# Optimization experiments

Hardware: AMD Instinct MI355X
Metric: run time of the kernel (lower is better)

Reference implementation:

```python
import jax, jax.numpy as jnp
import numpy as np

IMG_H, IMG_W = 512, 512
FEAT_HW = [64, 32, 16, 8, 4]
STRIDES = [8, 16, 32, 64, 128]
IN_CH = 256
NUM_ANCHORS = 9
NUM_CLASSES = 91
SCORE_THRESH = 0.05
NMS_THRESH = 0.5
TOPK = 1000            # batch_size_per_image
DETS = 300             # detections_per_image
BBOX_CLIP = float(np.log(1000.0 / 16.0))
PRIOR_P = 0.01


def _make_anchors():
    # torchvision-style grid anchors, 3 scales x 3 aspect ratios per location
    all_a = []
    for lvl, (hw, stride) in enumerate(zip(FEAT_HW, STRIDES)):
        base = 32.0 * (2.0 ** lvl)
        scales = np.array([1.0, 2.0 ** (1.0 / 3.0), 2.0 ** (2.0 / 3.0)])
        ratios = np.array([0.5, 1.0, 2.0])
        ws = (base * scales[None, :] / np.sqrt(ratios)[:, None]).reshape(-1)  # [9]
        hs = (base * scales[None, :] * np.sqrt(ratios)[:, None]).reshape(-1)
        shifts = (np.arange(hw) + 0.5) * stride
        cy, cx = np.meshgrid(shifts, shifts, indexing='ij')
        cx = cx.reshape(-1, 1)
        cy = cy.reshape(-1, 1)
        a = np.stack([cx - ws / 2, cy - hs / 2, cx + ws / 2, cy + hs / 2], axis=-1)  # [HW, 9, 4]
        all_a.append(a.reshape(-1, 4))
    return np.concatenate(all_a, axis=0).astype(np.float32)


def setup_inputs() -> dict:
    key = jax.random.key(0)
    ks = jax.random.split(key, 10)
    inp = {}
    for i, hw in enumerate(FEAT_HW):
        inp[f'feat{i}'] = jax.random.normal(ks[i], (1, IN_CH, hw, hw), jnp.float32)
    inp['anchors'] = jnp.asarray(_make_anchors())
    tower_std, out_std = 0.03, 0.01
    inp['cls_tower_w'] = jax.random.normal(ks[5], (4, IN_CH, IN_CH, 3, 3), jnp.float32) * tower_std
    inp['cls_tower_b'] = jnp.zeros((4, IN_CH), jnp.float32)
    inp['cls_logits_w'] = jax.random.normal(ks[6], (NUM_ANCHORS * NUM_CLASSES, IN_CH, 3, 3), jnp.float32) * out_std
    inp['cls_logits_b'] = jnp.full((NUM_ANCHORS * NUM_CLASSES,), -np.log((1.0 - PRIOR_P) / PRIOR_P), jnp.float32)
    inp['reg_tower_w'] = jax.random.normal(ks[7], (4, IN_CH, IN_CH, 3, 3), jnp.float32) * tower_std
    inp['reg_tower_b'] = jnp.zeros((4, IN_CH), jnp.float32)
    inp['reg_bbox_w'] = jax.random.normal(ks[8], (NUM_ANCHORS * 4, IN_CH, 3, 3), jnp.float32) * out_std
    inp['reg_bbox_b'] = jnp.zeros((NUM_ANCHORS * 4,), jnp.float32)
    return inp


def _conv3x3(x, w, b):
    y = jax.lax.conv_general_dilated(x, w, (1, 1), 'SAME', dimension_numbers=('NCHW', 'OIHW', 'NCHW'))
    return y + b[None, :, None, None]


def _head(x, tw, tb, ow, ob, out_ch):
    # 4-layer conv tower with ReLU, then output conv; reshape to [B, H*W*A, out_ch]
    for i in range(4):
        x = jax.nn.relu(_conv3x3(x, tw[i], tb[i]))
    y = _conv3x3(x, ow, ob)  # [B, A*out_ch, H, W]
    B, _, H, W = y.shape
    return y.reshape(B, NUM_ANCHORS, out_ch, H, W).transpose(0, 3, 4, 1, 2).reshape(B, H * W * NUM_ANCHORS, out_ch)


def _decode(rel, anc):
    # BoxCoder.decode_single with weights (1,1,1,1)
    w = anc[:, 2] - anc[:, 0]
    h = anc[:, 3] - anc[:, 1]
    cx = anc[:, 0] + 0.5 * w
    cy = anc[:, 1] + 0.5 * h
    dx, dy = rel[:, 0], rel[:, 1]
    dw = jnp.minimum(rel[:, 2], BBOX_CLIP)
    dh = jnp.minimum(rel[:, 3], BBOX_CLIP)
    pcx = dx * w + cx
    pcy = dy * h + cy
    pw = jnp.exp(dw) * w
    ph = jnp.exp(dh) * h
    return jnp.stack([pcx - 0.5 * pw, pcy - 0.5 * ph, pcx + 0.5 * pw, pcy + 0.5 * ph], axis=1)


def _level_candidates(logits, reg, anc):
    # logits [A_l, K], reg [A_l, 4], anc [A_l, 4]
    scores = jax.nn.sigmoid(logits).reshape(-1)          # [A_l*K]
    masked = jnp.where(scores > SCORE_THRESH, scores, -1.0)
    top_s, top_i = jax.lax.top_k(masked, TOPK)           # fixed-size topk; invalid -> -1
    labels = top_i % NUM_CLASSES
    a_idx = top_i // NUM_CLASSES
    boxes = _decode(reg[a_idx], anc[a_idx])
    boxes = jnp.stack([
        jnp.clip(boxes[:, 0], 0.0, float(IMG_W)), jnp.clip(boxes[:, 1], 0.0, float(IMG_H)),
        jnp.clip(boxes[:, 2], 0.0, float(IMG_W)), jnp.clip(boxes[:, 3], 0.0, float(IMG_H))], axis=1)
    return top_s, boxes, labels


def _nms_image(boxes, scores, labels):
    # batched_nms: offset boxes by label so different classes never overlap,
    # then greedy NMS with fixed DETS iterations (padded with invalid slots).
    NEG = jnp.float32(-1e9)
    off = labels.astype(boxes.dtype) * (jnp.max(boxes) + 1.0)
    b = boxes + off[:, None]
    area = (b[:, 2] - b[:, 0]) * (b[:, 3] - b[:, 1])
    alive0 = jnp.where(scores > SCORE_THRESH, scores, NEG)

    def step(alive, _):
        j = jnp.argmax(alive)
        valid = alive[j] > SCORE_THRESH
        bj = b[j]
        lt = jnp.maximum(bj[:2], b[:, :2])
        rb = jnp.minimum(bj[2:], b[:, 2:])
        wh = jnp.maximum(rb - lt, 0.0)
        inter = wh[:, 0] * wh[:, 1]
        iou = inter / (area[j] + area - inter + 1e-12)
        alive = jnp.where(iou > NMS_THRESH, NEG, alive).at[j].set(NEG)
        return alive, (j, valid)

    _, (sel, valid) = jax.lax.scan(step, alive0, None, length=DETS)
    out_s = jnp.where(valid, scores[sel], 0.0)
    out_b = jnp.where(valid[:, None], boxes[sel], 0.0)
    out_l = jnp.where(valid, labels[sel], -1)
    return out_s, out_b, out_l


def _forward(feats, anchors, ctw, ctb, cow, cob, rtw, rtb, row, rob):
    cand = []
    a_off = 0
    for f in feats:
        B, _, H, W = f.shape
        logits = _head(f, ctw, ctb, cow, cob, NUM_CLASSES)   # [B, HWA, K]
        reg = _head(f, rtw, rtb, row, rob, 4)                # [B, HWA, 4]
        a_l = H * W * NUM_ANCHORS
        anc = anchors[a_off:a_off + a_l]
        a_off += a_l
        cand.append(jax.vmap(_level_candidates, in_axes=(0, 0, None))(logits, reg, anc))
    scores = jnp.concatenate([c[0] for c in cand], axis=1)   # [B, 5*TOPK]
    boxes = jnp.concatenate([c[1] for c in cand], axis=1)    # [B, 5*TOPK, 4]
    labels = jnp.concatenate([c[2] for c in cand], axis=1)
    out_s, out_b, out_l = jax.vmap(_nms_image)(boxes, scores, labels)
    out = jnp.concatenate([out_s[..., None], out_b], axis=-1)  # [B, DETS, 5] = (score, x1, y1, x2, y2)
    return out, out_l


def reference(feat0, feat1, feat2, feat3, feat4, anchors, cls_tower_w, cls_tower_b,
              cls_logits_w, cls_logits_b, reg_tower_w, reg_tower_b, reg_bbox_w, reg_bbox_b):
    out, labels = _forward([feat0, feat1, feat2, feat3, feat4], anchors,
                           cls_tower_w, cls_tower_b, cls_logits_w, cls_logits_b,
                           reg_tower_w, reg_tower_b, reg_bbox_w, reg_bbox_b)
    return out, labels
```

## Files before the change

kernel.cpp:

```cpp
#include <hip/hip_runtime.h>
#include <hip/hip_bf16.h>
#include <math.h>

#define CIN 256
#define NUM_CLASSES 91
#define NUM_ANCH 9
#define KEY_CAP 65536
#define NCAND 5000
#define BBOX_CLIP_F 4.135166556742356f
#define CLS_THRESH 0.05f
#define PITCH 5456
#define PP_TOT 5972
#define PLANE_E 1528832
#define PLANE_B 3057664
#define ABUF_B  6115328
#define SLB     147456
#define LO_OFF  13312
#define PHASE   26624

typedef __attribute__((ext_vector_type(4))) float f4;
typedef _Float16 h8 __attribute__((ext_vector_type(8)));

#define MFMA(a,b,c) __builtin_amdgcn_mfma_f32_16x16x32_f16(a,b,c,0,0,0)

__constant__ int c_wsh[5]  = {6,5,4,3,2};
__constant__ int c_hw[5]   = {4096,1024,256,64,16};
__constant__ int c_wp[5]   = {66,34,18,10,6};
__constant__ int c_poff[5] = {0,4356,5512,5836,5936};
__constant__ int c_slen[5] = {198,136,108,100,36};
__constant__ int c_loff[5] = {0,4096,5120,5376,5440};
__constant__ int c_aoff[5] = {0,36864,46080,48384,48960};
__constant__ int s_cum[11] = {0,16,32,48,64,80,96,112,164,168,184};

__device__ __forceinline__ unsigned short f16r(float f) {
    _Float16 h = (_Float16)f;
    return __builtin_bit_cast(unsigned short, h);
}
__device__ __forceinline__ float f16tof(unsigned short u) {
    return (float)__builtin_bit_cast(_Float16, u);
}
__device__ __forceinline__ void split16(float v, unsigned short& h, unsigned short& l) {
    unsigned short hh = (fabsf(v) < 6.103515625e-05f) ? (unsigned short)0 : f16r(v);
    h = hh;
    l = f16r((v - f16tof(hh)) * 4096.0f);
}
__device__ __forceinline__ void gl_lds(const void* g, void* l) {
    __builtin_amdgcn_global_load_lds((const __attribute__((address_space(1))) void*)g,
                                     (__attribute__((address_space(3))) void*)l, 16, 0, 0);
}
__device__ __forceinline__ void tile_geom(int tile, int& lvl, int& px0, int& y0) {
    if (tile < 64)      { lvl = 0; px0 = tile << 6; y0 = tile; }
    else if (tile < 80) { lvl = 1; int j = tile - 64; px0 = j << 6; y0 = j << 1; }
    else if (tile < 84) { lvl = 2; int j = tile - 80; px0 = j << 6; y0 = j << 2; }
    else if (tile == 84){ lvl = 3; px0 = 0; y0 = 0; }
    else                { lvl = 4; px0 = 0; y0 = 0; }
}

__global__ void pad_k(const float* __restrict__ f0, const float* __restrict__ f1,
                      const float* __restrict__ f2, const float* __restrict__ f3,
                      const float* __restrict__ f4, unsigned short* __restrict__ IN) {
    int gid = blockIdx.x * 256 + threadIdx.x;
    if (gid >= 256 * PITCH) return;
    int cin = gid / PITCH, g = gid - cin * PITCH;
    int lvl = (g < 4096) ? 0 : (g < 5120) ? 1 : (g < 5376) ? 2 : (g < 5440) ? 3 : 4;
    const float* f = (lvl == 0) ? f0 : (lvl == 1) ? f1 : (lvl == 2) ? f2 : (lvl == 3) ? f3 : f4;
    int pix = g - c_loff[lvl];
    int wsh = c_wsh[lvl];
    int y = pix >> wsh, x = pix & ((1 << wsh) - 1);
    float v = f[(size_t)cin * c_hw[lvl] + pix];
    unsigned short h, l;
    split16(v, h, l);
    size_t idx = ((size_t)(cin >> 5) * PP_TOT + c_poff[lvl] + (size_t)(y + 1) * c_wp[lvl] + x + 1) * 32 + (cin & 31);
    IN[idx] = h;
    IN[PLANE_E + idx] = l;
}

__global__ void wprep_k(const float* __restrict__ ctw, const float* __restrict__ rtw,
                        const float* __restrict__ cow, const float* __restrict__ row_,
                        unsigned short* __restrict__ wf) {
    int gid = blockIdx.x * 256 + threadIdx.x;
    if (gid >= 184 * 72 * 64) return;
    int lane = gid & 63;
    int t = gid >> 6;
    int tap = t % 9;
    int t2 = t / 9;
    int chunk = t2 & 7;
    int cbg = t2 >> 3;
    int r = 0;
#pragma unroll
    for (int i = 1; i <= 10; ++i) if (cbg >= s_cum[i]) r = i;
    int cbl = cbg - s_cum[r];
    const float* src;
    int coutCnt;
    if (r < 3)       { src = ctw + (size_t)(r + 1) * 589824; coutCnt = 256; }
    else if (r < 7)  { src = rtw + (size_t)(r - 3) * 589824; coutCnt = 256; }
    else if (r == 7) { src = cow; coutCnt = 819; }
    else if (r == 8) { src = row_; coutCnt = 36; }
    else             { src = ctw; coutCnt = 256; }
    int cout = cbl * 16 + (lane & 15);
    int q = lane >> 4;
    unsigned short H[8], L[8];
#pragma unroll
    for (int j = 0; j < 8; ++j) {
        int cin = chunk * 32 + q * 8 + j;
        float v = (cout < coutCnt) ? src[((size_t)cout * 256 + cin) * 9 + tap] : 0.0f;
        split16(v, H[j], L[j]);
    }
    size_t off = (size_t)cbg * 73728 + (size_t)(chunk * 9 + tap) * 1024 + (size_t)lane * 8;
#pragma unroll
    for (int j = 0; j < 8; ++j) { wf[off + j] = H[j]; wf[off + 512 + j] = L[j]; }
}

__device__ __forceinline__ void kloop(const unsigned short* __restrict__ src,
        const char* __restrict__ wf0, char* sm, int wid, int lane,
        int s_base, int s_len, int Wp, const int sloc[2], f4 acc1[2][2], f4 acc2[2][2]) {
    const char* wp = wf0 + lane * 16;
    int nc = (s_len * 64 + 1023) >> 10;
    const char* gbase = (const char*)src;
    {
        const char* g = gbase + (size_t)s_base * 64;
        for (int c = wid; c < nc; c += 4) {
            gl_lds(g + (size_t)c * 1024 + (size_t)lane * 16, sm + c * 1024);
            gl_lds(g + PLANE_B + (size_t)c * 1024 + (size_t)lane * 16, sm + LO_OFF + c * 1024);
        }
    }
    h8 bh0 = *(const h8*)(wp);
    h8 bl0 = *(const h8*)(wp + 1024);
    h8 bh1 = *(const h8*)(wp + SLB);
    h8 bl1 = *(const h8*)(wp + SLB + 1024);
    __syncthreads();
    for (int chunk = 0; chunk < 8; ++chunk) {
        char* smc = sm + (chunk & 1) * PHASE;
        if (chunk < 7) {
            char* smn = sm + ((chunk & 1) ^ 1) * PHASE;
            const char* g = gbase + ((size_t)(chunk + 1) * PP_TOT + s_base) * 64;
            for (int c = wid; c < nc; c += 4) {
                gl_lds(g + (size_t)c * 1024 + (size_t)lane * 16, smn + c * 1024);
                gl_lds(g + PLANE_B + (size_t)c * 1024 + (size_t)lane * 16, smn + LO_OFF + c * 1024);
            }
        }
#pragma unroll
        for (int tap = 0; tap < 9; ++tap) {
            int kt = chunk * 9 + tap;
            int wo2 = ((kt < 71) ? kt + 1 : kt) * 2048;
            h8 nh0 = *(const h8*)(wp + wo2);
            h8 nl0 = *(const h8*)(wp + wo2 + 1024);
            h8 nh1 = *(const h8*)(wp + SLB + wo2);
            h8 nl1 = *(const h8*)(wp + SLB + wo2 + 1024);
            int toff = ((tap / 3) - 1) * Wp + (tap % 3) - 1;
            int so = toff * 64;
            h8 ah0 = *(const h8*)(smc + sloc[0] + so);
            h8 al0 = *(const h8*)(smc + LO_OFF + sloc[0] + so);
            h8 ah1 = *(const h8*)(smc + sloc[1] + so);
            h8 al1 = *(const h8*)(smc + LO_OFF + sloc[1] + so);
            acc1[0][0] = MFMA(ah0, bh0, acc1[0][0]);
            acc2[0][0] = MFMA(al0, bh0, acc2[0][0]);
            acc2[0][0] = MFMA(ah0, bl0, acc2[0][0]);
            acc1[1][0] = MFMA(ah1, bh0, acc1[1][0]);
            acc2[1][0] = MFMA(al1, bh0, acc2[1][0]);
            acc2[1][0] = MFMA(ah1, bl0, acc2[1][0]);
            acc1[0][1] = MFMA(ah0, bh1, acc1[0][1]);
            acc2[0][1] = MFMA(al0, bh1, acc2[0][1]);
            acc2[0][1] = MFMA(ah0, bl1, acc2[0][1]);
            acc1[1][1] = MFMA(ah1, bh1, acc1[1][1]);
            acc2[1][1] = MFMA(al1, bh1, acc2[1][1]);
            acc2[1][1] = MFMA(ah1, bl1, acc2[1][1]);
            bh0 = nh0; bl0 = nl0; bh1 = nh1; bl1 = nl1;
        }
        __syncthreads();
    }
}

__global__ __launch_bounds__(256, 3) void conv_t(
        const unsigned short* __restrict__ srcC, const unsigned short* __restrict__ srcR,
        unsigned short* __restrict__ dstC, unsigned short* __restrict__ dstR,
        const unsigned short* __restrict__ wfC, const unsigned short* __restrict__ wfR,
        const float* __restrict__ bC, const float* __restrict__ bR) {
    __shared__ __align__(16) char sm[2 * PHASE];
    int tid = threadIdx.x, lane = tid & 63, wid = tid >> 6;
    int quad = lane >> 4, l16 = lane & 15;
    int bx = blockIdx.x;
    int cb = bx & 3, tower = (bx >> 2) & 1, tile = bx >> 3;
    const unsigned short* src = tower ? srcR : srcC;
    unsigned short* dst = tower ? dstR : dstC;
    const unsigned short* wfx = tower ? wfR : wfC;
    const float* bias = tower ? bR : bC;

    int lvl, px0, y0;
    tile_geom(tile, lvl, px0, y0);
    int wsh = c_wsh[lvl], HW = c_hw[lvl], Wp = c_wp[lvl];
    int poff = c_poff[lvl];
    int s_base = poff + y0 * Wp, s_len = c_slen[lvl];
    int Mh = (wid & 1) * 32, Nh32 = wid >> 1;

    int sloc[2];
#pragma unroll
    for (int mb = 0; mb < 2; ++mb) {
        int p = px0 + Mh + mb * 16 + l16;
        if (p >= HW) p = HW - 1;
        int y = p >> wsh, x = p & ((1 << wsh) - 1);
        sloc[mb] = ((y - y0 + 1) * Wp + x + 1) * 64 + quad * 16;
    }
    f4 acc1[2][2], acc2[2][2];
#pragma unroll
    for (int mb = 0; mb < 2; ++mb)
#pragma unroll
        for (int sl = 0; sl < 2; ++sl) { acc1[mb][sl] = (f4)0.0f; acc2[mb][sl] = (f4)0.0f; }

    const char* wf0 = (const char*)wfx + (size_t)(cb * 4 + Nh32 * 2) * SLB;
    kloop(src, wf0, sm, wid, lane, s_base, s_len, Wp, sloc, acc1, acc2);

    int cbase = cb * 64 + Nh32 * 32;
    float bv[2];
    bv[0] = bias[cbase + l16];
    bv[1] = bias[cbase + 16 + l16];
#pragma unroll
    for (int mb = 0; mb < 2; ++mb) {
        int pb = px0 + Mh + mb * 16 + quad * 4;
#pragma unroll
        for (int r = 0; r < 4; ++r) {
            int p = pb + r;
            bool valid = p < HW;
            int pc = valid ? p : 0;
            int y = pc >> wsh, x = pc & ((1 << wsh) - 1);
            size_t ppix = poff + (size_t)(y + 1) * Wp + x + 1;
#pragma unroll
            for (int sl = 0; sl < 2; ++sl) {
                int coutg = cbase + sl * 16 + l16;
                float v = fmaf(acc2[mb][sl][r], 0.000244140625f, acc1[mb][sl][r]) + bv[sl];
                v = fmaxf(v, 0.0f);
                unsigned short h, l;
                split16(v, h, l);
                size_t idx = ((size_t)(coutg >> 5) * PP_TOT + ppix) * 32 + (coutg & 31);
                if (valid) { dst[idx] = h; dst[PLANE_E + idx] = l; }
            }
        }
    }
}

__global__ __launch_bounds__(256, 3) void mhead_t(
        const unsigned short* __restrict__ srcC, const unsigned short* __restrict__ srcR,
        const unsigned short* __restrict__ wfCls, const unsigned short* __restrict__ wfReg,
        const float* __restrict__ cob, const float* __restrict__ rob,
        unsigned long long* __restrict__ keys, int* __restrict__ cnt,
        float* __restrict__ regout) {
    __shared__ __align__(16) char sm[2 * PHASE];
    int tid = threadIdx.x, lane = tid & 63, wid = tid >> 6;
    int quad = lane >> 4, l16 = lane & 15;
    int bx = blockIdx.x, tile = bx / 14, sub = bx - tile * 14;
    bool isCls = sub < 13;

    int lvl, px0, y0;
    tile_geom(tile, lvl, px0, y0);
    int wsh = c_wsh[lvl], HW = c_hw[lvl], Wp = c_wp[lvl];
    int poff = c_poff[lvl];
    int s_base = poff + y0 * Wp, s_len = c_slen[lvl];
    int Mh = (wid & 1) * 32, Nh32 = wid >> 1;

    int sloc[2];
#pragma unroll
    for (int mb = 0; mb < 2; ++mb) {
        int p = px0 + Mh + mb * 16 + l16;
        if (p >= HW) p = HW - 1;
        int y = p >> wsh, x = p & ((1 << wsh) - 1);
        sloc[mb] = ((y - y0 + 1) * Wp + x + 1) * 64 + quad * 16;
    }
    f4 acc1[2][2], acc2[2][2];
#pragma unroll
    for (int mb = 0; mb < 2; ++mb)
#pragma unroll
        for (int sl = 0; sl < 2; ++sl) { acc1[mb][sl] = (f4)0.0f; acc2[mb][sl] = (f4)0.0f; }

    const unsigned short* src = isCls ? srcC : srcR;
    const char* wf0 = isCls ? (const char*)wfCls + (size_t)(sub * 4 + Nh32 * 2) * SLB
                            : (const char*)wfReg + (size_t)(Nh32 * 2) * SLB;
    kloop(src, wf0, sm, wid, lane, s_base, s_len, Wp, sloc, acc1, acc2);

    if (isCls) {
        int chb = sub * 64 + Nh32 * 32;
        float cbv[2];
#pragma unroll
        for (int sl = 0; sl < 2; ++sl) {
            int ch = chb + sl * 16 + l16;
            cbv[sl] = (ch < 819) ? cob[ch] : 0.0f;
        }
#pragma unroll
        for (int mb = 0; mb < 2; ++mb) {
            int pb = px0 + Mh + mb * 16 + quad * 4;
#pragma unroll
            for (int r = 0; r < 4; ++r) {
                int p = pb + r;
                bool valid = p < HW;
#pragma unroll
                for (int sl = 0; sl < 2; ++sl) {
                    int ch = chb + sl * 16 + l16;
                    if (valid && ch < 819) {
                        float lg = fmaf(acc2[mb][sl][r], 0.000244140625f, acc1[mb][sl][r]) + cbv[sl];
                        float s = 1.0f / (1.0f + expf(-lg));
                        if (s > CLS_THRESH) {
                            int a = ch / NUM_CLASSES;
                            int cls = ch - a * NUM_CLASSES;
                            unsigned flat = (unsigned)((p * NUM_ANCH + a) * NUM_CLASSES + cls);
                            int pos = atomicAdd(cnt + lvl, 1);
                            if (pos < KEY_CAP)
                                keys[(size_t)lvl * KEY_CAP + pos] =
                                    ((unsigned long long)__float_as_uint(s) << 32) |
                                    (unsigned long long)(~flat);
                        }
                    }
                }
            }
        }
    } else {
        int chb = Nh32 * 32;
        float rbv[2];
#pragma unroll
        for (int sl = 0; sl < 2; ++sl) {
            int ch = chb + sl * 16 + l16;
            rbv[sl] = (ch < 36) ? rob[ch] : 0.0f;
        }
        int loff = c_loff[lvl];
#pragma unroll
        for (int mb = 0; mb < 2; ++mb) {
            int pb = px0 + Mh + mb * 16 + quad * 4;
#pragma unroll
            for (int r = 0; r < 4; ++r) {
                int p = pb + r;
                bool valid = p < HW;
#pragma unroll
                for (int sl = 0; sl < 2; ++sl) {
                    int ch = chb + sl * 16 + l16;
                    if (valid && ch < 36)
                        regout[(size_t)ch * PITCH + loff + p] =
                            fmaf(acc2[mb][sl][r], 0.000244140625f, acc1[mb][sl][r]) + rbv[sl];
                }
            }
        }
    }
}

__global__ __launch_bounds__(1024) void sort5_k(unsigned long long* keys, const int* cnt) {
    const int lvl = blockIdx.x;
    unsigned long long* kb = keys + (size_t)lvl * KEY_CAP;
    int n = cnt[lvl]; if (n > KEY_CAP) n = KEY_CAP;
    int m = 2; while (m < n) m <<= 1;
    __shared__ unsigned long long sk[8192];
    if (m <= 8192) {
        for (int i = threadIdx.x; i < m; i += 1024) sk[i] = (i < n) ? kb[i] : 0ull;
        __syncthreads();
        for (int k = 2; k <= m; k <<= 1)
            for (int j = k >> 1; j > 0; j >>= 1) {
                for (int i = threadIdx.x; i < m; i += 1024) {
                    int ixj = i ^ j;
                    if (ixj > i) {
                        unsigned long long a = sk[i], b = sk[ixj];
                        bool desc = (i & k) == 0;
                        if (desc ? (a < b) : (a > b)) { sk[i] = b; sk[ixj] = a; }
                    }
                }
                __syncthreads();
            }
        for (int i = threadIdx.x; i < m; i += 1024) kb[i] = sk[i];
    } else {
        for (int i = threadIdx.x; i < m; i += 1024) if (i >= n) kb[i] = 0ull;
        __syncthreads();
        for (int k = 2; k <= m; k <<= 1)
            for (int j = k >> 1; j > 0; j >>= 1) {
                for (int i = threadIdx.x; i < m; i += 1024) {
                    int ixj = i ^ j;
                    if (ixj > i) {
                        unsigned long long a = kb[i], b = kb[ixj];
                        bool desc = (i & k) == 0;
                        if (desc ? (a < b) : (a > b)) { kb[i] = b; kb[ixj] = a; }
                    }
                }
                __syncthreads();
            }
    }
}

__global__ void emit_k(const unsigned long long* __restrict__ keys, const int* __restrict__ cnt,
                       const float* __restrict__ regout, const float* __restrict__ anchors,
                       float* __restrict__ cs, float* __restrict__ cb, int* __restrict__ cl) {
#pragma clang fp contract(off)
    int r = blockIdx.x * 256 + threadIdx.x;
    if (r >= NCAND) return;
    int lvl = r / 1000, rr = r - lvl * 1000;
    int n = cnt[lvl]; if (n > KEY_CAP) n = KEY_CAP; if (n > 1000) n = 1000;
    float score = -1.0f, b0 = 0.f, b1 = 0.f, b2 = 0.f, b3 = 0.f;
    int label = 0;
    if (rr < n) {
        unsigned long long key = keys[(size_t)lvl * KEY_CAP + rr];
        score = __uint_as_float((unsigned)(key >> 32));
        unsigned flat = ~((unsigned)(key & 0xFFFFFFFFull));
        label = (int)(flat % NUM_CLASSES);
        int af = (int)(flat / NUM_CLASSES);
        int a = af % NUM_ANCH;
        int pix = af / NUM_ANCH;
        int gp = c_loff[lvl] + pix;
        float dx = regout[(size_t)(a * 4 + 0) * PITCH + gp];
        float dy = regout[(size_t)(a * 4 + 1) * PITCH + gp];
        float dw = regout[(size_t)(a * 4 + 2) * PITCH + gp];
        float dh = regout[(size_t)(a * 4 + 3) * PITCH + gp];
        const float* an = anchors + (size_t)(c_aoff[lvl] + af) * 4;
        float aw = an[2] - an[0];
        float ah = an[3] - an[1];
        float cx = an[0] + 0.5f * aw;
        float cy = an[1] + 0.5f * ah;
        dw = fminf(dw, BBOX_CLIP_F);
        dh = fminf(dh, BBOX_CLIP_F);
        float pcx = dx * aw + cx;
        float pcy = dy * ah + cy;
        float pw = expf(dw) * aw;
        float ph = expf(dh) * ah;
        b0 = fminf(fmaxf(pcx - 0.5f * pw, 0.0f), 512.0f);
        b1 = fminf(fmaxf(pcy - 0.5f * ph, 0.0f), 512.0f);
        b2 = fminf(fmaxf(pcx + 0.5f * pw, 0.0f), 512.0f);
        b3 = fminf(fmaxf(pcy + 0.5f * ph, 0.0f), 512.0f);
    }
    cs[r] = score;
    cb[(size_t)r * 4 + 0] = b0;
    cb[(size_t)r * 4 + 1] = b1;
    cb[(size_t)r * 4 + 2] = b2;
    cb[(size_t)r * 4 + 3] = b3;
    cl[r] = label;
}

__global__ void rank_k(const float* __restrict__ cs, const float* __restrict__ cbx,
                       const int* __restrict__ cl, const int* __restrict__ cnt,
                       int* __restrict__ order, float* __restrict__ sbox,
                       float* __restrict__ sarea, int* __restrict__ nvp) {
#pragma clang fp contract(off)
    __shared__ int vls[5];
    int t = blockIdx.x * 256 + threadIdx.x;
    if (threadIdx.x < 5) {
        int n = cnt[threadIdx.x]; if (n > 1000) n = 1000;
        vls[threadIdx.x] = n;
    }
    __syncthreads();
    if (t >= NCAND) return;
    if (t == 0) *nvp = vls[0] + vls[1] + vls[2] + vls[3] + vls[4];
    int lvl = t / 1000, pos = t - lvl * 1000;
    if (pos >= vls[lvl]) return;
    float s = cs[t];
    int rank = pos;
#pragma unroll
    for (int l2 = 0; l2 < 5; ++l2) {
        if (l2 == lvl) continue;
        int n = vls[l2];
        const float* seg = cs + l2 * 1000;
        int lo = 0, hi = n;
        if (l2 < lvl) {
            while (lo < hi) { int mid = (lo + hi) >> 1; if (seg[mid] >= s) lo = mid + 1; else hi = mid; }
        } else {
            while (lo < hi) { int mid = (lo + hi) >> 1; if (seg[mid] > s) lo = mid + 1; else hi = mid; }
        }
        rank += lo;
    }
    order[rank] = t;
    float off = (float)cl[t] * 513.0f;
    float x1 = cbx[(size_t)t * 4 + 0] + off;
    float y1 = cbx[(size_t)t * 4 + 1] + off;
    float x2 = cbx[(size_t)t * 4 + 2] + off;
    float y2 = cbx[(size_t)t * 4 + 3] + off;
    sbox[(size_t)rank * 4 + 0] = x1;
    sbox[(size_t)rank * 4 + 1] = y1;
    sbox[(size_t)rank * 4 + 2] = x2;
    sbox[(size_t)rank * 4 + 3] = y2;
    sarea[rank] = (x2 - x1) * (y2 - y1);
}

__global__ void mask_k(const float* __restrict__ sbox, const float* __restrict__ sarea,
                       const int* __restrict__ nvp, unsigned long long* __restrict__ mask) {
#pragma clang fp contract(off)
    int nv = *nvp;
    int t = blockIdx.x * 256 + threadIdx.x;
    if (t >= NCAND * 80) return;
    int i = t / 80, w = t - i * 80;
    if (i >= nv) return;
    float ix1 = sbox[(size_t)i * 4 + 0];
    float iy1 = sbox[(size_t)i * 4 + 1];
    float ix2 = sbox[(size_t)i * 4 + 2];
    float iy2 = sbox[(size_t)i * 4 + 3];
    float ai = sarea[i];
    unsigned long long bits = 0ull;
    int j0 = w * 64;
    for (int b = 0; b < 64; ++b) {
        int j = j0 + b;
        if (j < nv) {
            float jx1 = sbox[(size_t)j * 4 + 0];
            float jy1 = sbox[(size_t)j * 4 + 1];
            float jx2 = sbox[(size_t)j * 4 + 2];
            float jy2 = sbox[(size_t)j * 4 + 3];
            float aj = sarea[j];
            float ltx = fmaxf(ix1, jx1), lty = fmaxf(iy1, jy1);
            float rbx = fminf(ix2, jx2), rby = fminf(iy2, jy2);
            float wx = fmaxf(rbx - ltx, 0.0f), wy = fmaxf(rby - lty, 0.0f);
            float inter = wx * wy;
            float iou = inter / (ai + aj - inter + 1e-12f);
            if (iou > 0.5f) bits |= (1ull << b);
        }
    }
    mask[(size_t)i * 80 + w] = bits;
}

__global__ __launch_bounds__(64) void sweep_k(const unsigned long long* __restrict__ mask,
        const int* __restrict__ nvp, int* __restrict__ accbuf, int* __restrict__ naccp) {
    const int l = threadIdx.x;
    int nv = *nvp; if (nv > NCAND) nv = NCAND;
    int nacc = 0;
    if (nv > 0) {
        unsigned long long sup0 = 0ull, sup1 = 0ull;
        int ntiles = (nv + 63) >> 6;
        bool done = false;
        for (int g0 = 0; g0 < ntiles && !done; g0 += 8) {
            int gcnt = ntiles - g0; if (gcnt > 8) gcnt = 8;
            unsigned long long ml[8];
#pragma unroll
            for (int g = 0; g < 8; ++g) {
                int t = g0 + g;
                int row = (t << 6) + l;
                ml[g] = (g < gcnt && row < nv) ? mask[(size_t)row * 80 + t] : 0ull;
            }
            for (int g = 0; g < gcnt && !done; ++g) {
                int t = g0 + g;
                unsigned long long cur = (t < 64)
                    ? (unsigned long long)__shfl((long long)sup0, t, 64)
                    : (unsigned long long)__shfl((long long)sup1, t - 64, 64);
                int lim = nv - (t << 6);
                unsigned long long valid = (lim >= 64) ? ~0ull : ((1ull << lim) - 1ull);
                unsigned long long rem = ~cur & valid;
                unsigned long long Aset = 0ull;
                while (rem) {
                    int k = __builtin_ctzll(rem);
                    Aset |= 1ull << k;
                    if (l == 0) accbuf[nacc] = (t << 6) + k;
                    ++nacc;
                    if (nacc == 300) { done = true; break; }
                    unsigned long long mlk = (unsigned long long)__shfl((long long)ml[g], k, 64);
                    cur |= mlk | (1ull << k);
                    rem = ~cur & valid;
                }
                if (!done) {
                    unsigned long long t2 = Aset;
                    while (t2) {
                        int i0 = __builtin_ctzll(t2); t2 &= t2 - 1;
                        int i1 = -1, i2 = -1, i3 = -1;
                        if (t2) { i1 = __builtin_ctzll(t2); t2 &= t2 - 1; }
                        if (t2) { i2 = __builtin_ctzll(t2); t2 &= t2 - 1; }
                        if (t2) { i3 = __builtin_ctzll(t2); t2 &= t2 - 1; }
                        size_t r0 = (size_t)((t << 6) + i0) * 80;
                        unsigned long long w0 = mask[r0 + l];
                        unsigned long long w1 = (i1 >= 0) ? mask[(size_t)((t << 6) + i1) * 80 + l] : 0ull;
                        unsigned long long w2 = (i2 >= 0) ? mask[(size_t)((t << 6) + i2) * 80 + l] : 0ull;
                        unsigned long long w3 = (i3 >= 0) ? mask[(size_t)((t << 6) + i3) * 80 + l] : 0ull;
                        sup0 |= w0 | w1 | w2 | w3;
                        if (l < 16) {
                            unsigned long long v0 = mask[r0 + 64 + l];
                            unsigned long long v1 = (i1 >= 0) ? mask[(size_t)((t << 6) + i1) * 80 + 64 + l] : 0ull;
                            unsigned long long v2 = (i2 >= 0) ? mask[(size_t)((t << 6) + i2) * 80 + 64 + l] : 0ull;
                            unsigned long long v3 = (i3 >= 0) ? mask[(size_t)((t << 6) + i3) * 80 + 64 + l] : 0ull;
                            sup1 |= v0 | v1 | v2 | v3;
                        }
                    }
                }
            }
        }
    }
    if (l == 0) *naccp = nacc;
}

__global__ void fill_k(const float* __restrict__ cs, const float* __restrict__ cb,
                       const int* __restrict__ cl, const int* __restrict__ order,
                       const int* __restrict__ accbuf, const int* __restrict__ naccp,
                       float* __restrict__ out) {
    int t = blockIdx.x * 64 + threadIdx.x;
    if (t >= 300) return;
    int na = *naccp;
    if (t < na) {
        int c = order[accbuf[t]];
        out[t * 5 + 0] = cs[c];
        out[t * 5 + 1] = cb[(size_t)c * 4 + 0];
        out[t * 5 + 2] = cb[(size_t)c * 4 + 1];
        out[t * 5 + 3] = cb[(size_t)c * 4 + 2];
        out[t * 5 + 4] = cb[(size_t)c * 4 + 3];
        out[1500 + t] = (float)cl[c];
    } else {
        out[t * 5 + 0] = 0.0f; out[t * 5 + 1] = 0.0f; out[t * 5 + 2] = 0.0f;
        out[t * 5 + 3] = 0.0f; out[t * 5 + 4] = 0.0f;
        out[1500 + t] = -1.0f;
    }
}

extern "C" void kernel_launch(void* const* d_in, const int* in_sizes, int n_in,
                              void* d_out, int out_size, void* d_ws, size_t ws_size,
                              hipStream_t stream) {
    const float* f0 = (const float*)d_in[0];
    const float* f1 = (const float*)d_in[1];
    const float* f2 = (const float*)d_in[2];
    const float* f3 = (const float*)d_in[3];
    const float* f4 = (const float*)d_in[4];
    const float* anchors = (const float*)d_in[5];
    const float* ctw = (const float*)d_in[6];
    const float* ctb = (const float*)d_in[7];
    const float* cow = (const float*)d_in[8];
    const float* cob = (const float*)d_in[9];
    const float* rtw = (const float*)d_in[10];
    const float* rtb = (const float*)d_in[11];
    const float* row_ = (const float*)d_in[12];
    const float* rob = (const float*)d_in[13];
    float* out = (float*)d_out;

    char* base = (char*)d_ws;
    unsigned short* wf = (unsigned short*)base;
    unsigned short* C  = (unsigned short*)(base + 24772608);
    unsigned short* IN = (unsigned short*)(base + 30887936);
    unsigned short* A  = (unsigned short*)(base + 37003264);
    unsigned short* B  = (unsigned short*)(base + 43118592);
    int* cnt           = (int*)(base + 49233920);
    int* nvp           = cnt + 6;
    int* naccp         = cnt + 7;
    float* cs    = (float*)(base + 0);
    float* cbx   = (float*)(base + 32768);
    int*   cl    = (int*)(base + 131072);
    int*   order = (int*)(base + 163840);
    float* sbox  = (float*)(base + 262144);
    float* sarea = (float*)(base + 344064);
    int*   accbuf = (int*)(base + 368640);
    unsigned long long* keys = (unsigned long long*)A;
    float* regout            = (float*)(base + 37003264 + 2621440);
    unsigned long long* mask = (unsigned long long*)B;

    unsigned short* SL_clsL[4] = {wf + (size_t)168 * 73728, wf + (size_t)0 * 73728,
                                  wf + (size_t)16 * 73728,  wf + (size_t)32 * 73728};
    unsigned short* SL_regL[4] = {wf + (size_t)48 * 73728, wf + (size_t)64 * 73728,
                                  wf + (size_t)80 * 73728, wf + (size_t)96 * 73728};
    unsigned short* SL_clsH = wf + (size_t)112 * 73728;
    unsigned short* SL_regH = wf + (size_t)164 * 73728;

    hipMemsetAsync(C, 0, 4 * (size_t)ABUF_B, stream);
    hipMemsetAsync(cnt, 0, 32, stream);

    pad_k<<<(256 * PITCH + 255) / 256, 256, 0, stream>>>(f0, f1, f2, f3, f4, IN);
    wprep_k<<<(184 * 72 * 64 + 255) / 256, 256, 0, stream>>>(ctw, rtw, cow, row_, wf);

    conv_t<<<86 * 8, 256, 0, stream>>>(IN, IN, A, B, SL_clsL[0], SL_regL[0], ctb, rtb);
    hipMemsetAsync(C, 0, (size_t)ABUF_B, stream);
    conv_t<<<86 * 8, 256, 0, stream>>>(A, B, C, IN, SL_clsL[1], SL_regL[1], ctb + 256, rtb + 256);
    conv_t<<<86 * 8, 256, 0, stream>>>(C, IN, A, B, SL_clsL[2], SL_regL[2], ctb + 512, rtb + 512);
    conv_t<<<86 * 8, 256, 0, stream>>>(A, B, C, IN, SL_clsL[3], SL_regL[3], ctb + 768, rtb + 768);

    mhead_t<<<86 * 14, 256, 0, stream>>>(C, IN, SL_clsH, SL_regH, cob, rob, keys, cnt, regout);

    sort5_k<<<5, 1024, 0, stream>>>(keys, cnt);
    emit_k<<<(NCAND + 255) / 256, 256, 0, stream>>>(keys, cnt, regout, anchors, cs, cbx, cl);
    rank_k<<<(NCAND + 255) / 256, 256, 0, stream>>>(cs, cbx, cl, cnt, order, sbox, sarea, nvp);
    mask_k<<<(NCAND * 80 + 255) / 256, 256, 0, stream>>>(sbox, sarea, nvp, mask);
    sweep_k<<<1, 64, 0, stream>>>(mask, nvp, accbuf, naccp);
    fill_k<<<5, 64, 0, stream>>>(cs, cbx, cl, order, accbuf, naccp, out);
}
```

Before: 528.2 us.

## Stage only high fp16 plane in LDS, load low plane directly from global

The split-fp16 conv kernels no longer stage the low-half activation plane in shared memory. Each lane now prefetches its low-half A fragments straight from global memory, one tap ahead. This halves the LDS footprint per block, and launch bounds are raised from 3 to 4 blocks per CU to use the freed space for occupancy. The trade-off is more uncoalesced global/L2 traffic for the low plane and added register pressure from the extra prefetch registers.

```diff
diff --git a/kernel.cpp b/kernel.cpp
--- a/kernel.cpp
+++ b/kernel.cpp
@@ -15,8 +15,7 @@
 #define PLANE_B 3057664
 #define ABUF_B  6115328
 #define SLB     147456
-#define LO_OFF  13312
-#define PHASE   26624
+#define HPHASE  13312
 
 typedef __attribute__((ext_vector_type(4))) float f4;
 typedef _Float16 h8 __attribute__((ext_vector_type(8)));
@@ -112,33 +111,38 @@
 }
 
 __device__ __forceinline__ void kloop(const unsigned short* __restrict__ src,
-        const char* __restrict__ wf0, char* sm, int wid, int lane,
-        int s_base, int s_len, int Wp, const int sloc[2], f4 acc1[2][2], f4 acc2[2][2]) {
+        const char* __restrict__ wf0, char* sm, int wid, int lane, int quad,
+        int s_base, int s_len, int Wp, const int relrow[2], f4 acc1[2][2], f4 acc2[2][2]) {
     const char* wp = wf0 + lane * 16;
     int nc = (s_len * 64 + 1023) >> 10;
     const char* gbase = (const char*)src;
     {
         const char* g = gbase + (size_t)s_base * 64;
-        for (int c = wid; c < nc; c += 4) {
+        for (int c = wid; c < nc; c += 4)
             gl_lds(g + (size_t)c * 1024 + (size_t)lane * 16, sm + c * 1024);
-            gl_lds(g + PLANE_B + (size_t)c * 1024 + (size_t)lane * 16, sm + LO_OFF + c * 1024);
-        }
-    }
+    }
+    const char* lo0 = gbase + PLANE_B + (size_t)(s_base + relrow[0]) * 64 + quad * 16;
+    const char* lo1 = gbase + PLANE_B + (size_t)(s_base + relrow[1]) * 64 + quad * 16;
+    const int t00 = (-1 - Wp) * 64;
     h8 bh0 = *(const h8*)(wp);
     h8 bl0 = *(const h8*)(wp + 1024);
     h8 bh1 = *(const h8*)(wp + SLB);
     h8 bl1 = *(const h8*)(wp + SLB + 1024);
+    h8 al0 = *(const h8*)(lo0 + t00);
+    h8 al1 = *(const h8*)(lo1 + t00);
     __syncthreads();
+    int sA0 = relrow[0] * 64 + (quad << 4);
+    int sA1 = relrow[1] * 64 + (quad << 4);
     for (int chunk = 0; chunk < 8; ++chunk) {
-        char* smc = sm + (chunk & 1) * PHASE;
+        char* smc = sm + (chunk & 1) * HPHASE;
         if (chunk < 7) {
-            char* smn = sm + ((chunk & 1) ^ 1) * PHASE;
+            char* smn = sm + ((chunk & 1) ^ 1) * HPHASE;
             const char* g = gbase + ((size_t)(chunk + 1) * PP_TOT + s_base) * 64;
-            for (int c = wid; c < nc; c += 4) {
+            for (int c = wid; c < nc; c += 4)
                 gl_lds(g + (size_t)c * 1024 + (size_t)lane * 16, smn + c * 1024);
-                gl_lds(g + PLANE_B + (size_t)c * 1024 + (size_t)lane * 16, smn + LO_OFF + c * 1024);
-            }
-        }
+        }
+        const char* lo0n = (chunk < 7) ? lo0 + (size_t)PP_TOT * 64 : lo0;
+        const char* lo1n = (chunk < 7) ? lo1 + (size_t)PP_TOT * 64 : lo1;
 #pragma unroll
         for (int tap = 0; tap < 9; ++tap) {
             int kt = chunk * 9 + tap;
@@ -147,12 +151,18 @@
             h8 nl0 = *(const h8*)(wp + wo2 + 1024);
             h8 nh1 = *(const h8*)(wp + SLB + wo2);
             h8 nl1 = *(const h8*)(wp + SLB + wo2 + 1024);
-            int toff = ((tap / 3) - 1) * Wp + (tap % 3) - 1;
-            int so = toff * 64;
-            h8 ah0 = *(const h8*)(smc + sloc[0] + so);
-            h8 al0 = *(const h8*)(smc + LO_OFF + sloc[0] + so);
-            h8 ah1 = *(const h8*)(smc + sloc[1] + so);
-            h8 al1 = *(const h8*)(smc + LO_OFF + sloc[1] + so);
+            h8 na0, na1;
+            if (tap < 8) {
+                int tn = (((tap + 1) / 3) - 1) * Wp + ((tap + 1) % 3) - 1;
+                na0 = *(const h8*)(lo0 + tn * 64);
+                na1 = *(const h8*)(lo1 + tn * 64);
+            } else {
+                na0 = *(const h8*)(lo0n + t00);
+                na1 = *(const h8*)(lo1n + t00);
+            }
+            int so = (((tap / 3) - 1) * Wp + (tap % 3) - 1) * 64;
+            h8 ah0 = *(const h8*)(smc + sA0 + so);
+            h8 ah1 = *(const h8*)(smc + sA1 + so);
             acc1[0][0] = MFMA(ah0, bh0, acc1[0][0]);
             acc2[0][0] = MFMA(al0, bh0, acc2[0][0]);
             acc2[0][0] = MFMA(ah0, bl0, acc2[0][0]);
@@ -166,17 +176,19 @@
             acc2[1][1] = MFMA(al1, bh1, acc2[1][1]);
             acc2[1][1] = MFMA(ah1, bl1, acc2[1][1]);
             bh0 = nh0; bl0 = nl0; bh1 = nh1; bl1 = nl1;
-        }
+            al0 = na0; al1 = na1;
+        }
+        lo0 = lo0n; lo1 = lo1n;
         __syncthreads();
     }
 }
 
-__global__ __launch_bounds__(256, 3) void conv_t(
+__global__ __launch_bounds__(256, 4) void conv_t(
         const unsigned short* __restrict__ srcC, const unsigned short* __restrict__ srcR,
         unsigned short* __restrict__ dstC, unsigned short* __restrict__ dstR,
         const unsigned short* __restrict__ wfC, const unsigned short* __restrict__ wfR,
         const float* __restrict__ bC, const float* __restrict__ bR) {
-    __shared__ __align__(16) char sm[2 * PHASE];
+    __shared__ __align__(16) char sm[2 * HPHASE];
     int tid = threadIdx.x, lane = tid & 63, wid = tid >> 6;
     int quad = lane >> 4, l16 = lane & 15;
     int bx = blockIdx.x;
@@ -193,13 +205,13 @@
     int s_base = poff + y0 * Wp, s_len = c_slen[lvl];
     int Mh = (wid & 1) * 32, Nh32 = wid >> 1;
 
-    int sloc[2];
+    int relrow[2];
 #pragma unroll
     for (int mb = 0; mb < 2; ++mb) {
         int p = px0 + Mh + mb * 16 + l16;
         if (p >= HW) p = HW - 1;
         int y = p >> wsh, x = p & ((1 << wsh) - 1);
-        sloc[mb] = ((y - y0 + 1) * Wp + x + 1) * 64 + quad * 16;
+        relrow[mb] = (y - y0 + 1) * Wp + x + 1;
     }
     f4 acc1[2][2], acc2[2][2];
 #pragma unroll
@@ -208,7 +220,7 @@
         for (int sl = 0; sl < 2; ++sl) { acc1[mb][sl] = (f4)0.0f; acc2[mb][sl] = (f4)0.0f; }
 
     const char* wf0 = (const char*)wfx + (size_t)(cb * 4 + Nh32 * 2) * SLB;
-    kloop(src, wf0, sm, wid, lane, s_base, s_len, Wp, sloc, acc1, acc2);
+    kloop(src, wf0, sm, wid, lane, quad, s_base, s_len, Wp, relrow, acc1, acc2);
 
     int cbase = cb * 64 + Nh32 * 32;
     float bv[2];
@@ -238,13 +250,13 @@
     }
 }
 
-__global__ __launch_bounds__(256, 3) void mhead_t(
+__global__ __launch_bounds__(256, 4) void mhead_t(
         const unsigned short* __restrict__ srcC, const unsigned short* __restrict__ srcR,
         const unsigned short* __restrict__ wfCls, const unsigned short* __restrict__ wfReg,
         const float* __restrict__ cob, const float* __restrict__ rob,
         unsigned long long* __restrict__ keys, int* __restrict__ cnt,
         float* __restrict__ regout) {
-    __shared__ __align__(16) char sm[2 * PHASE];
+    __shared__ __align__(16) char sm[2 * HPHASE];
     int tid = threadIdx.x, lane = tid & 63, wid = tid >> 6;
     int quad = lane >> 4, l16 = lane & 15;
     int bx = blockIdx.x, tile = bx / 14, sub = bx - tile * 14;
@@ -257,13 +269,13 @@
     int s_base = poff + y0 * Wp, s_len = c_slen[lvl];
     int Mh = (wid & 1) * 32, Nh32 = wid >> 1;
 
-    int sloc[2];
+    int relrow[2];
 #pragma unroll
     for (int mb = 0; mb < 2; ++mb) {
         int p = px0 + Mh + mb * 16 + l16;
         if (p >= HW) p = HW - 1;
         int y = p >> wsh, x = p & ((1 << wsh) - 1);
-        sloc[mb] = ((y - y0 + 1) * Wp + x + 1) * 64 + quad * 16;
+        relrow[mb] = (y - y0 + 1) * Wp + x + 1;
     }
     f4 acc1[2][2], acc2[2][2];
 #pragma unroll
@@ -274,7 +286,7 @@
     const unsigned short* src = isCls ? srcC : srcR;
     const char* wf0 = isCls ? (const char*)wfCls + (size_t)(sub * 4 + Nh32 * 2) * SLB
                             : (const char*)wfReg + (size_t)(Nh32 * 2) * SLB;
-    kloop(src, wf0, sm, wid, lane, s_base, s_len, Wp, sloc, acc1, acc2);
+    kloop(src, wf0, sm, wid, lane, quad, s_base, s_len, Wp, relrow, acc1, acc2);
 
     if (isCls) {
         int chb = sub * 64 + Nh32 * 32;
```

Result: slower. 617.6 us (+16.9%).
